# Kernel optimization log

Measured on AMD Instinct MI355X. Metric: run time of the kernel, lower is better.

## Reference

```python
import jax, jax.numpy as jnp
import numpy as np

B, T, D, H, FF = 4, 2048, 768, 12, 4
DH = D // H


def _ln(x, g, b, eps=1e-5):
    mu = x.mean(-1, keepdims=True)
    var = ((x - mu) ** 2).mean(-1, keepdims=True)
    return (x - mu) * jax.lax.rsqrt(var + eps) * g + b


def setup_inputs() -> dict:
    key = jax.random.key(0)
    ks = jax.random.split(key, 16)
    s = 0.02
    d = {
        'x': jax.random.normal(ks[0], (B, T, D), jnp.float32),
        'Wq': jax.random.normal(ks[1], (D, D), jnp.float32) * s,
        'bq': jnp.zeros((D,), jnp.float32),
        'Wk': jax.random.normal(ks[2], (D, D), jnp.float32) * s,
        'bk': jnp.zeros((D,), jnp.float32),
        'Wv': jax.random.normal(ks[3], (D, D), jnp.float32) * s,
        'bv': jnp.zeros((D,), jnp.float32),
        'Wo': jax.random.normal(ks[4], (D, D), jnp.float32) * s,
        'bo': jnp.zeros((D,), jnp.float32),
        'W1': jax.random.normal(ks[5], (D, D * FF), jnp.float32) * s,
        'b1': jnp.zeros((D * FF,), jnp.float32),
        'W2': jax.random.normal(ks[6], (D * FF, D), jnp.float32) * s,
        'b2': jnp.zeros((D,), jnp.float32),
        'g1': jnp.ones((D,), jnp.float32),
        'be1': jnp.zeros((D,), jnp.float32),
        'g2': jnp.ones((D,), jnp.float32),
        'be2': jnp.zeros((D,), jnp.float32),
        'radius': 64,
    }
    return d


def reference(x, Wq, bq, Wk, bk, Wv, bv, Wo, bo, W1, b1, W2, b2, g1, be1, g2, be2, radius):
    Bc, Tc, Dc = x.shape
    # local mask: blocked (True) where |i-j| > radius (clamping in torch code is a no-op)
    i = jnp.arange(Tc)
    mask = jnp.abs(i[:, None] - i[None, :]) > radius  # [T,T] True = masked

    h = _ln(x, g1, be1)
    q = (h @ Wq + bq).reshape(Bc, Tc, H, DH)
    k = (h @ Wk + bk).reshape(Bc, Tc, H, DH)
    v = (h @ Wv + bv).reshape(Bc, Tc, H, DH)
    scale = 1.0 / jnp.sqrt(jnp.asarray(DH, x.dtype))
    scores = jnp.einsum('bthd,bshd->bhts', q, k) * scale  # [B,H,T,T]
    scores = jnp.where(mask[None, None], -jnp.inf, scores)
    attn = jax.nn.softmax(scores, axis=-1)
    ctx = jnp.einsum('bhts,bshd->bthd', attn, v).reshape(Bc, Tc, Dc)
    x = x + (ctx @ Wo + bo)

    h2 = _ln(x, g2, be2)
    ff = jax.nn.gelu(h2 @ W1 + b1, approximate=False) @ W2 + b2
    return x + ff
```

## Files before the change

### kernel.cpp

```cpp
#include <hip/hip_runtime.h>
#include <hip/hip_bf16.h>

#define B_  4
#define T_  2048
#define D_  768
#define H_  12
#define DH_ 64
#define FF_ 3072

typedef __attribute__((ext_vector_type(8))) short bf16x8;
typedef __attribute__((ext_vector_type(4))) float f32x4;
typedef __attribute__((ext_vector_type(4))) unsigned short us4;

#define MFMA16(a, b, c) __builtin_amdgcn_mfma_f32_16x16x32_bf16((a), (b), (c), 0, 0, 0)

__device__ __forceinline__ unsigned short f2bf(float f) {
    union { float f; unsigned u; } v; v.f = f;
    unsigned r = v.u + 0x7fffu + ((v.u >> 16) & 1u);
    return (unsigned short)(r >> 16);
}
__device__ __forceinline__ float bf2f(unsigned short s) {
    union { unsigned u; float f; } v; v.u = ((unsigned)s) << 16;
    return v.f;
}

__device__ __forceinline__ float gelu_fast(float v) {
    const float u2 = 2.0f * v * fmaf(0.0356774081f, v * v, 0.7978845608f);
    const float e = __expf(u2);
    const float r = __builtin_amdgcn_rcpf(e + 1.0f);
    const float th = fmaf(-2.0f, r, 1.0f);
    return 0.5f * v * (1.0f + th);
}

__device__ __forceinline__ void gload_lds16(const unsigned short* gp, unsigned short* lp) {
    __builtin_amdgcn_global_load_lds(
        (const __attribute__((address_space(1))) unsigned int*)gp,
        (__attribute__((address_space(3))) unsigned int*)lp,
        16, 0, 0);
}

__global__ __launch_bounds__(256) void tcvt_kernel(
    const float* __restrict__ src, unsigned short* __restrict__ dst, int K, int N)
{
    __shared__ float tile[32][33];
    const int bx = blockIdx.x * 32;
    const int by = blockIdx.y * 32;
    const int tx = threadIdx.x, ty = threadIdx.y;
#pragma unroll
    for (int i = 0; i < 32; i += 8)
        tile[ty + i][tx] = src[(size_t)(by + ty + i) * N + bx + tx];
    __syncthreads();
#pragma unroll
    for (int i = 0; i < 32; i += 8)
        dst[(size_t)(bx + ty + i) * K + by + tx] = f2bf(tile[tx][ty + i]);
}

__global__ __launch_bounds__(256) void tcvt4_kernel(
    const float* __restrict__ s0, const float* __restrict__ s1,
    const float* __restrict__ s2, const float* __restrict__ s3,
    unsigned short* __restrict__ dst)
{
    __shared__ float tile[32][33];
    const int z = blockIdx.z;
    const float* src = (z == 0) ? s0 : (z == 1) ? s1 : (z == 2) ? s2 : s3;
    unsigned short* d = dst + (size_t)z * 589824;
    const int bx = blockIdx.x * 32;
    const int by = blockIdx.y * 32;
    const int tx = threadIdx.x, ty = threadIdx.y;
#pragma unroll
    for (int i = 0; i < 32; i += 8)
        tile[ty + i][tx] = src[(size_t)(by + ty + i) * 768 + bx + tx];
    __syncthreads();
#pragma unroll
    for (int i = 0; i < 32; i += 8)
        d[(size_t)(bx + ty + i) * 768 + by + tx] = f2bf(tile[tx][ty + i]);
}

__global__ __launch_bounds__(256) void ln_kernel(
    const float* __restrict__ x, const float* __restrict__ g,
    const float* __restrict__ be, unsigned short* __restrict__ out)
{
    const int lane = threadIdx.x & 63;
    const int row = blockIdx.x * 4 + (threadIdx.x >> 6);
    const float4* xr = (const float4*)(x + (size_t)row * D_);
    float4 v0 = xr[lane], v1 = xr[lane + 64], v2 = xr[lane + 128];
    float s  = v0.x + v0.y + v0.z + v0.w + v1.x + v1.y + v1.z + v1.w
             + v2.x + v2.y + v2.z + v2.w;
    float s2 = v0.x*v0.x + v0.y*v0.y + v0.z*v0.z + v0.w*v0.w
             + v1.x*v1.x + v1.y*v1.y + v1.z*v1.z + v1.w*v1.w
             + v2.x*v2.x + v2.y*v2.y + v2.z*v2.z + v2.w*v2.w;
#pragma unroll
    for (int o = 1; o < 64; o <<= 1) {
        s  += __shfl_xor(s,  o);
        s2 += __shfl_xor(s2, o);
    }
    const float mu = s * (1.0f / D_);
    const float var = s2 * (1.0f / D_) - mu * mu;
    const float rstd = rsqrtf(var + 1e-5f);
    const float4* gv = (const float4*)g;
    const float4* bv = (const float4*)be;
    us4* orow = (us4*)(out + (size_t)row * D_);
#pragma unroll
    for (int k = 0; k < 3; ++k) {
        const float4 v = (k == 0) ? v0 : (k == 1) ? v1 : v2;
        const float4 gg = gv[lane + k * 64];
        const float4 bb = bv[lane + k * 64];
        us4 p;
        p[0] = f2bf((v.x - mu) * rstd * gg.x + bb.x);
        p[1] = f2bf((v.y - mu) * rstd * gg.y + bb.y);
        p[2] = f2bf((v.z - mu) * rstd * gg.z + bb.z);
        p[3] = f2bf((v.w - mu) * rstd * gg.w + bb.w);
        orow[lane + k * 64] = p;
    }
}

__global__ __launch_bounds__(256) void reduce_ln_kernel(
    const unsigned short* __restrict__ p0, const unsigned short* __restrict__ p1,
    const float* __restrict__ x, const float* __restrict__ bo,
    const float* __restrict__ g, const float* __restrict__ be,
    float* __restrict__ x2, unsigned short* __restrict__ h2)
{
    const int row = blockIdx.x;
    const int t = threadIdx.x;
    const size_t base = (size_t)row * D_;
    float v[3];
    float s = 0.0f, s2 = 0.0f;
#pragma unroll
    for (int j = 0; j < 3; ++j) {
        const int c = t + j * 256;
        const float vv = bf2f(p0[base + c]) + bf2f(p1[base + c]) + bo[c] + x[base + c];
        v[j] = vv;
        x2[base + c] = vv;
        s += vv; s2 += vv * vv;
    }
#pragma unroll
    for (int o = 1; o < 64; o <<= 1) {
        s  += __shfl_xor(s,  o);
        s2 += __shfl_xor(s2, o);
    }
    __shared__ float rs[4], rq[4];
    const int wave = t >> 6;
    if ((t & 63) == 0) { rs[wave] = s; rq[wave] = s2; }
    __syncthreads();
    s  = rs[0] + rs[1] + rs[2] + rs[3];
    s2 = rq[0] + rq[1] + rq[2] + rq[3];
    const float mu = s * (1.0f / D_);
    const float var = s2 * (1.0f / D_) - mu * mu;
    const float rstd = rsqrtf(var + 1e-5f);
#pragma unroll
    for (int j = 0; j < 3; ++j) {
        const int c = t + j * 256;
        h2[base + c] = f2bf((v[j] - mu) * rstd * g[c] + be[c]);
    }
}

__global__ __launch_bounds__(256) void reduce_out_kernel(
    const unsigned short* __restrict__ p0, const unsigned short* __restrict__ p1,
    const float* __restrict__ x2, const float* __restrict__ b2,
    float* __restrict__ out)
{
    const int n4 = B_ * T_ * D_ / 4;
    for (int i = blockIdx.x * 256 + threadIdx.x; i < n4; i += gridDim.x * 256) {
        const us4 a = ((const us4*)p0)[i];
        const us4 b = ((const us4*)p1)[i];
        const float4 xr = ((const float4*)x2)[i];
        const int col = (i * 4) % D_;
        float4 o;
        o.x = bf2f(a[0]) + bf2f(b[0]) + b2[col]     + xr.x;
        o.y = bf2f(a[1]) + bf2f(b[1]) + b2[col + 1] + xr.y;
        o.z = bf2f(a[2]) + bf2f(b[2]) + b2[col + 2] + xr.z;
        o.w = bf2f(a[3]) + bf2f(b[3]) + b2[col + 3] + xr.w;
        ((float4*)out)[i] = o;
    }
}

template<int MODE>
__global__ __launch_bounds__(256, 3) void gemm4w(
    const unsigned short* __restrict__ A,
    const unsigned short* __restrict__ Bt,
    const float* __restrict__ bias,
    const float* __restrict__ bias2,
    const float* __restrict__ bias3,
    void* __restrict__ outp,
    void* __restrict__ out2,
    void* __restrict__ out3,
    int N, int K, int kLen, int nTilesN, int nTilesMN, long partStride)
{
    __shared__ __align__(16) unsigned short As[128 * 64];
    __shared__ __align__(16) unsigned short Bs[128 * 64];

    const int nwg = gridDim.x;
    const int q = nwg >> 3, rr = nwg & 7;
    const int xcd = blockIdx.x & 7, loc = blockIdx.x >> 3;
    const int swz = (xcd < rr ? xcd * (q + 1) : rr * (q + 1) + (xcd - rr) * q) + loc;
    const int ks  = swz / nTilesMN;
    const int rem = swz - ks * nTilesMN;
    const int m0 = (rem / nTilesN) * 128;
    const int n0 = (rem % nTilesN) * 128;
    const int kOff = ks * kLen;

    const int tid = threadIdx.x;
    const int wv = tid >> 6;
    const int lane = tid & 63;
    const int wr = wv >> 1;
    const int wc = wv & 1;

    f32x4 zero4 = {0.0f, 0.0f, 0.0f, 0.0f};
    f32x4 acc[4][4];
#pragma unroll
    for (int i = 0; i < 4; ++i)
#pragma unroll
        for (int j = 0; j < 4; ++j) acc[i][j] = zero4;

    const int lrow = lane >> 3;
    const int scb = (lane & 7) ^ lrow;
    const unsigned short* ag = A  + (size_t)(m0 + wv * 32 + lrow) * K + kOff + scb * 8;
    const unsigned short* bg = Bt + (size_t)(n0 + wv * 32 + lrow) * K + kOff + scb * 8;
    unsigned short* aLds = As + wv * 32 * 64;
    unsigned short* bLds = Bs + wv * 32 * 64;

    const int fr = lane & 15;
    const int fg = lane >> 4;
    const int sw = fr & 7;
    const int aRow = (wr * 64 + fr) * 64;
    const int bRow = (wc * 64 + fr) * 64;

    const int nk = kLen >> 6;
    for (int kt = 0; kt < nk; ++kt) {
        const int k0 = kt << 6;
        __syncthreads();
#pragma unroll
        for (int c = 0; c < 4; ++c)
            gload_lds16(ag + k0 + (size_t)c * 8 * K, aLds + c * 512);
#pragma unroll
        for (int c = 0; c < 4; ++c)
            gload_lds16(bg + k0 + (size_t)c * 8 * K, bLds + c * 512);
        __syncthreads();

#pragma unroll
        for (int kk = 0; kk < 2; ++kk) {
            bf16x8 afr[4], bfr[4];
            const int cb = ((kk * 4 + fg) ^ sw) << 3;
#pragma unroll
            for (int mm = 0; mm < 4; ++mm)
                afr[mm] = *(const bf16x8*)(As + aRow + mm * 1024 + cb);
#pragma unroll
            for (int nn = 0; nn < 4; ++nn)
                bfr[nn] = *(const bf16x8*)(Bs + bRow + nn * 1024 + cb);
#pragma unroll
            for (int mm = 0; mm < 4; ++mm)
#pragma unroll
                for (int nn = 0; nn < 4; ++nn)
                    acc[mm][nn] = MFMA16(afr[mm], bfr[nn], acc[mm][nn]);
        }
    }

    const int lc = lane & 15;
    const int lr = (lane >> 4) * 4;
#pragma unroll
    for (int mm = 0; mm < 4; ++mm) {
        const int gm0 = m0 + wr * 64 + mm * 16 + lr;
#pragma unroll
        for (int nn = 0; nn < 4; ++nn) {
            const int gn = n0 + wc * 64 + nn * 16 + lc;
            if (MODE == 4) {
                if (gn < 1536) {
                    const float bv = (gn < 768) ? bias[gn] : bias2[gn - 768];
                    unsigned short* o = (gn < 768) ? (unsigned short*)outp : (unsigned short*)out2;
                    const int col = (gn < 768) ? gn : gn - 768;
#pragma unroll
                    for (int r = 0; r < 4; ++r)
                        o[(size_t)(gm0 + r) * 768 + col] = f2bf(acc[mm][nn][r] + bv);
                } else {
                    const float bv = bias3[gn - 1536];
                    const int b = gm0 / T_;
                    const int tl = gm0 - b * T_;
                    us4 pk;
#pragma unroll
                    for (int r = 0; r < 4; ++r) pk[r] = f2bf(acc[mm][nn][r] + bv);
                    *(us4*)((unsigned short*)out3 + ((size_t)(b * D_ + gn - 1536)) * T_ + tl) = pk;
                }
            } else if (MODE == 5) {
                unsigned short* o = (unsigned short*)outp + (size_t)ks * partStride;
#pragma unroll
                for (int r = 0; r < 4; ++r)
                    o[(size_t)(gm0 + r) * N + gn] = f2bf(acc[mm][nn][r]);
            } else {
                const float bv = bias[gn];
#pragma unroll
                for (int r = 0; r < 4; ++r) {
                    const int gm = gm0 + r;
                    float v = acc[mm][nn][r] + bv;
                    if (MODE == 0) {
                        ((unsigned short*)outp)[(size_t)gm * N + gn] = f2bf(v);
                    } else if (MODE == 2) {
                        ((unsigned short*)outp)[(size_t)gm * N + gn] = f2bf(gelu_fast(v));
                    }
                }
            }
        }
    }
}

__global__ __launch_bounds__(256) void attn_kernel(
    const unsigned short* __restrict__ Q,
    const unsigned short* __restrict__ Kg,
    const unsigned short* __restrict__ Vt,
    unsigned short* __restrict__ ctx)
{
    __shared__ __align__(16) unsigned short Qs[64][72];
    __shared__ __align__(16) unsigned short KP[192 * 72];
    __shared__ __align__(16) unsigned short Vts[64][200];

    const int tid = threadIdx.x;
    const int lane = tid & 63;
    const int w = tid >> 6;
    const int bid = blockIdx.x;
    const int qt = bid & 31;
    const int h = (bid >> 5) % H_;
    const int b = bid / (32 * H_);
    const int qs = qt * 64;
    const int t0 = qs >= 64 ? qs - 64 : 0;
    const int t1 = (qs + 128 < T_) ? qs + 128 : T_;
    const int KW = t1 - t0;

    for (int s = tid; s < 512; s += 256) {
        const int r = s >> 3, c8 = (s & 7) << 3;
        *(uint4*)&Qs[r][c8] =
            *(const uint4*)&Q[((size_t)(b * T_ + qs + r)) * D_ + h * DH_ + c8];
    }
    unsigned short* Ks = KP;
    for (int s = tid; s < 1536; s += 256) {
        const int r = s >> 3, c8 = (s & 7) << 3;
        uint4 val = {0, 0, 0, 0};
        if (r < KW)
            val = *(const uint4*)&Kg[((size_t)(b * T_ + t0 + r)) * D_ + h * DH_ + c8];
        *(uint4*)&Ks[r * 72 + c8] = val;
    }
    for (int s = tid; s < 1536; s += 256) {
        const int r = s / 24, c8 = (s % 24) << 3;
        uint4 val = {0, 0, 0, 0};
        if (c8 < KW)
            val = *(const uint4*)&Vt[((size_t)((b * H_ + h) * DH_ + r)) * T_ + t0 + c8];
        *(uint4*)&Vts[r][c8] = val;
    }
    __syncthreads();

    f32x4 zero4 = {0.0f, 0.0f, 0.0f, 0.0f};
    f32x4 sa[12];
#pragma unroll
    for (int i = 0; i < 12; ++i) sa[i] = zero4;
#pragma unroll
    for (int ks = 0; ks < 2; ++ks) {
        const bf16x8 aq = *(const bf16x8*)&Qs[w * 16 + (lane & 15)][ks * 32 + (lane >> 4) * 8];
#pragma unroll
        for (int cf = 0; cf < 12; ++cf) {
            const bf16x8 bk = *(const bf16x8*)&Ks[(cf * 16 + (lane & 15)) * 72 + ks * 32 + (lane >> 4) * 8];
            sa[cf] = MFMA16(aq, bk, sa[cf]);
        }
    }
    __syncthreads();

    const int lq = w * 16 + (lane >> 4) * 4;
    float mx[4] = {-1e30f, -1e30f, -1e30f, -1e30f};
#pragma unroll
    for (int cf = 0; cf < 12; ++cf) {
        const int key = t0 + cf * 16 + (lane & 15);
#pragma unroll
        for (int r = 0; r < 4; ++r) {
            const int dd = (qs + lq + r) - key;
            const bool ok = (key < t1) && (dd <= 64) && (dd >= -64);
            const float sv = ok ? sa[cf][r] * 0.125f : -1e30f;
            sa[cf][r] = sv;
            mx[r] = fmaxf(mx[r], sv);
        }
    }
#pragma unroll
    for (int r = 0; r < 4; ++r)
#pragma unroll
        for (int o = 1; o < 16; o <<= 1)
            mx[r] = fmaxf(mx[r], __shfl_xor(mx[r], o));

    unsigned short* Ps = KP;
    float sm[4] = {0.0f, 0.0f, 0.0f, 0.0f};
#pragma unroll
    for (int cf = 0; cf < 12; ++cf) {
#pragma unroll
        for (int r = 0; r < 4; ++r) {
            const float p = __expf(sa[cf][r] - mx[r]);
            sm[r] += p;
            Ps[(lq + r) * 200 + cf * 16 + (lane & 15)] = f2bf(p);
        }
    }
#pragma unroll
    for (int r = 0; r < 4; ++r)
#pragma unroll
        for (int o = 1; o < 16; o <<= 1)
            sm[r] += __shfl_xor(sm[r], o);

    f32x4 oa[4];
#pragma unroll
    for (int i = 0; i < 4; ++i) oa[i] = zero4;
#pragma unroll
    for (int ks = 0; ks < 6; ++ks) {
        const bf16x8 ap = *(const bf16x8*)&Ps[(w * 16 + (lane & 15)) * 200 + ks * 32 + (lane >> 4) * 8];
#pragma unroll
        for (int nf = 0; nf < 4; ++nf) {
            const bf16x8 bv = *(const bf16x8*)&Vts[nf * 16 + (lane & 15)][ks * 32 + (lane >> 4) * 8];
            oa[nf] = MFMA16(ap, bv, oa[nf]);
        }
    }
#pragma unroll
    for (int nf = 0; nf < 4; ++nf) {
#pragma unroll
        for (int r = 0; r < 4; ++r) {
            const float o = oa[nf][r] / sm[r];
            ctx[((size_t)(b * T_ + qs + lq + r)) * D_ + h * DH_ + nf * 16 + (lane & 15)] = f2bf(o);
        }
    }
}

extern "C" void kernel_launch(void* const* d_in, const int* in_sizes, int n_in,
                              void* d_out, int out_size, void* d_ws, size_t ws_size,
                              hipStream_t stream)
{
    const float* x   = (const float*)d_in[0];
    const float* Wq  = (const float*)d_in[1];
    const float* bq  = (const float*)d_in[2];
    const float* Wk  = (const float*)d_in[3];
    const float* bk  = (const float*)d_in[4];
    const float* Wv  = (const float*)d_in[5];
    const float* bv  = (const float*)d_in[6];
    const float* Wo  = (const float*)d_in[7];
    const float* bo  = (const float*)d_in[8];
    const float* W1  = (const float*)d_in[9];
    const float* b1  = (const float*)d_in[10];
    const float* W2  = (const float*)d_in[11];
    const float* b2  = (const float*)d_in[12];
    const float* g1  = (const float*)d_in[13];
    const float* be1 = (const float*)d_in[14];
    const float* g2  = (const float*)d_in[15];
    const float* be2 = (const float*)d_in[16];
    float* out = (float*)d_out;

    unsigned short* wqkv_t = (unsigned short*)d_ws;
    unsigned short* wo_t = wqkv_t + 3 * 589824;
    unsigned short* w1_t = wo_t + 589824;
    unsigned short* w2_t = w1_t + 2359296;
    unsigned short* hbuf = w2_t + 2359296;
    unsigned short* qbuf = hbuf + 6291456;
    float* x2 = (float*)(qbuf + 6291456);
    unsigned short* kbuf = (unsigned short*)(x2 + 6291456);
    unsigned short* vtb  = kbuf + 6291456;
    unsigned short* ffb  = kbuf;

    dim3 tb(32, 8);
    tcvt4_kernel<<<dim3(24, 24, 4), tb, 0, stream>>>(Wq, Wk, Wv, Wo, wqkv_t);
    tcvt_kernel<<<dim3(96, 24), tb, 0, stream>>>(W1, w1_t, 768, 3072);
    tcvt_kernel<<<dim3(24, 96), tb, 0, stream>>>(W2, w2_t, 3072, 768);

    ln_kernel<<<2048, 256, 0, stream>>>(x, g1, be1, hbuf);

    gemm4w<4><<<64 * 18, 256, 0, stream>>>(
        hbuf, wqkv_t, bq, bk, bv, qbuf, kbuf, vtb, 2304, 768, 768, 18, 64 * 18, 0);

    attn_kernel<<<1536, 256, 0, stream>>>(qbuf, kbuf, vtb, hbuf);

    gemm4w<5><<<64 * 6 * 2, 256, 0, stream>>>(
        hbuf, wo_t, nullptr, nullptr, nullptr, kbuf, nullptr, nullptr,
        768, 768, 384, 6, 64 * 6, 6291456);

    reduce_ln_kernel<<<8192, 256, 0, stream>>>(
        kbuf, kbuf + 6291456, x, bo, g2, be2, x2, qbuf);

    gemm4w<2><<<64 * 24, 256, 0, stream>>>(
        qbuf, w1_t, b1, nullptr, nullptr, ffb, nullptr, nullptr,
        3072, 768, 768, 24, 64 * 24, 0);

    gemm4w<5><<<64 * 6 * 2, 256, 0, stream>>>(
        ffb, w2_t, nullptr, nullptr, nullptr, hbuf, nullptr, nullptr,
        768, 3072, 1536, 6, 64 * 6, 6291456);

    reduce_out_kernel<<<2048, 256, 0, stream>>>(
        hbuf, hbuf + 6291456, x2, b2, out);
}
```

Measured before the change: 230.7 us.

## Store residual in bf16, vectorize reduce-LN per wave, stage V transpose through LDS

The post-attention reduce+LayerNorm kernel now handles one row per wave with vectorized loads and stores, and drops the cross-wave shared-memory reduction. The intermediate residual x2 is stored as bf16 instead of fp32, which halves its write and read traffic in both reduce kernels. In the QKV GEMM, the V-transpose epilogue stages tiles in swizzled LDS so it can write coalesced 16-byte rows, replacing scattered 8-byte stores. Storing the residual in bf16 loses precision in the final output's residual path.

Result: faster. 223.1 us (-3.3%).

```diff
diff --git a/kernel.cpp b/kernel.cpp
--- a/kernel.cpp
+++ b/kernel.cpp
@@ -11,6 +11,7 @@
 typedef __attribute__((ext_vector_type(8))) short bf16x8;
 typedef __attribute__((ext_vector_type(4))) float f32x4;
 typedef __attribute__((ext_vector_type(4))) unsigned short us4;
+typedef __attribute__((ext_vector_type(8))) unsigned short us8;
 
 #define MFMA16(a, b, c) __builtin_amdgcn_mfma_f32_16x16x32_bf16((a), (b), (c), 0, 0, 0)
 
@@ -118,58 +119,70 @@
     const unsigned short* __restrict__ p0, const unsigned short* __restrict__ p1,
     const float* __restrict__ x, const float* __restrict__ bo,
     const float* __restrict__ g, const float* __restrict__ be,
-    float* __restrict__ x2, unsigned short* __restrict__ h2)
-{
-    const int row = blockIdx.x;
-    const int t = threadIdx.x;
+    unsigned short* __restrict__ x2, unsigned short* __restrict__ h2)
+{
+    const int lane = threadIdx.x & 63;
+    const int row = blockIdx.x * 4 + (threadIdx.x >> 6);
     const size_t base = (size_t)row * D_;
-    float v[3];
+    float v[12];
     float s = 0.0f, s2 = 0.0f;
 #pragma unroll
-    for (int j = 0; j < 3; ++j) {
-        const int c = t + j * 256;
-        const float vv = bf2f(p0[base + c]) + bf2f(p1[base + c]) + bo[c] + x[base + c];
-        v[j] = vv;
-        x2[base + c] = vv;
-        s += vv; s2 += vv * vv;
+    for (int k = 0; k < 3; ++k) {
+        const int c = k * 256 + lane * 4;
+        const us4 a = *(const us4*)(p0 + base + c);
+        const us4 b = *(const us4*)(p1 + base + c);
+        const float4 xr = *(const float4*)(x + base + c);
+        const float4 bb = *(const float4*)(bo + c);
+        const float w0 = bf2f(a[0]) + bf2f(b[0]) + bb.x + xr.x;
+        const float w1 = bf2f(a[1]) + bf2f(b[1]) + bb.y + xr.y;
+        const float w2 = bf2f(a[2]) + bf2f(b[2]) + bb.z + xr.z;
+        const float w3 = bf2f(a[3]) + bf2f(b[3]) + bb.w + xr.w;
+        v[k * 4 + 0] = w0; v[k * 4 + 1] = w1; v[k * 4 + 2] = w2; v[k * 4 + 3] = w3;
+        s += w0 + w1 + w2 + w3;
+        s2 += w0 * w0 + w1 * w1 + w2 * w2 + w3 * w3;
     }
 #pragma unroll
     for (int o = 1; o < 64; o <<= 1) {
         s  += __shfl_xor(s,  o);
         s2 += __shfl_xor(s2, o);
     }
-    __shared__ float rs[4], rq[4];
-    const int wave = t >> 6;
-    if ((t & 63) == 0) { rs[wave] = s; rq[wave] = s2; }
-    __syncthreads();
-    s  = rs[0] + rs[1] + rs[2] + rs[3];
-    s2 = rq[0] + rq[1] + rq[2] + rq[3];
     const float mu = s * (1.0f / D_);
     const float var = s2 * (1.0f / D_) - mu * mu;
     const float rstd = rsqrtf(var + 1e-5f);
 #pragma unroll
-    for (int j = 0; j < 3; ++j) {
-        const int c = t + j * 256;
-        h2[base + c] = f2bf((v[j] - mu) * rstd * g[c] + be[c]);
+    for (int k = 0; k < 3; ++k) {
+        const int c = k * 256 + lane * 4;
+        const float4 gg = *(const float4*)(g + c);
+        const float4 bb = *(const float4*)(be + c);
+        us4 xo, ho;
+        xo[0] = f2bf(v[k*4+0]); xo[1] = f2bf(v[k*4+1]);
+        xo[2] = f2bf(v[k*4+2]); xo[3] = f2bf(v[k*4+3]);
+        ho[0] = f2bf((v[k*4+0] - mu) * rstd * gg.x + bb.x);
+        ho[1] = f2bf((v[k*4+1] - mu) * rstd * gg.y + bb.y);
+        ho[2] = f2bf((v[k*4+2] - mu) * rstd * gg.z + bb.z);
+        ho[3] = f2bf((v[k*4+3] - mu) * rstd * gg.w + bb.w);
+        *(us4*)(x2 + base + c) = xo;
+        *(us4*)(h2 + base + c) = ho;
     }
 }
 
 __global__ __launch_bounds__(256) void reduce_out_kernel(
     const unsigned short* __restrict__ p0, const unsigned short* __restrict__ p1,
-    const float* __restrict__ x2, const float* __restrict__ b2,
+    const unsigned short* __restrict__ x2, const float* __restrict__ b2,
     float* __restrict__ out)
 {
     const int n4 = B_ * T_ * D_ / 4;
     for (int i = blockIdx.x * 256 + threadIdx.x; i < n4; i += gridDim.x * 256) {
         const us4 a = ((const us4*)p0)[i];
         const us4 b = ((const us4*)p1)[i];
-        const float4 xr = ((const float4*)x2)[i];
+        const us4 xr = ((const us4*)x2)[i];
         const int col = (i * 4) % D_;
+        const float4 bb = *(const float4*)(b2 + col);
         float4 o;
-        o.x = bf2f(a[0]) + bf2f(b[0]) + b2[col]     + xr.x;
-        o.y = bf2f(a[1]) + bf2f(b[1]) + b2[col + 1] + xr.y;
-        o.z = bf2f(a[2]) + bf2f(b[2]) + b2[col + 2] + xr.z;
-        o.w = bf2f(a[3]) + bf2f(b[3]) + b2[col + 3] + xr.w;
+        o.x = bf2f(a[0]) + bf2f(b[0]) + bb.x + bf2f(xr[0]);
+        o.y = bf2f(a[1]) + bf2f(b[1]) + bb.y + bf2f(xr[1]);
+        o.z = bf2f(a[2]) + bf2f(b[2]) + bb.z + bf2f(xr[2]);
+        o.w = bf2f(a[3]) + bf2f(b[3]) + bb.w + bf2f(xr[3]);
         ((float4*)out)[i] = o;
     }
 }
@@ -257,6 +270,39 @@
 
     const int lc = lane & 15;
     const int lr = (lane >> 4) * 4;
+
+    if (MODE == 4 && n0 >= 1536) {
+        __syncthreads();
+        unsigned short* Vl = As + wv * 4096;
+#pragma unroll
+        for (int mm = 0; mm < 4; ++mm) {
+            const int s = mm * 4 + (lane >> 4);
+            const int sp = s >> 1, so = s & 1;
+#pragma unroll
+            for (int nn = 0; nn < 4; ++nn) {
+                const int d = nn * 16 + lc;
+                const float bv = bias3[(n0 - 1536) + wc * 64 + d];
+                us4 pk;
+#pragma unroll
+                for (int r = 0; r < 4; ++r) pk[r] = f2bf(acc[mm][nn][r] + bv);
+                *(us4*)(Vl + d * 64 + ((sp ^ (d & 7)) << 3) + so * 4) = pk;
+            }
+        }
+        asm volatile("s_waitcnt lgkmcnt(0)" ::: "memory");
+        const int bb = m0 >> 11;
+        const int tl0 = (m0 & 2047) + wr * 64;
+        const size_t rowbase = (size_t)(bb * D_ + (n0 - 1536) + wc * 64);
+        unsigned short* vout = (unsigned short*)out3;
+#pragma unroll
+        for (int it = 0; it < 8; ++it) {
+            const int d = (lane >> 3) + it * 8;
+            const int c = lane & 7;
+            const us8 v = *(const us8*)(Vl + d * 64 + ((c ^ (d & 7)) << 3));
+            *(us8*)(vout + (rowbase + d) * (size_t)T_ + tl0 + c * 8) = v;
+        }
+        return;
+    }
+
 #pragma unroll
     for (int mm = 0; mm < 4; ++mm) {
         const int gm0 = m0 + wr * 64 + mm * 16 + lr;
@@ -264,22 +310,13 @@
         for (int nn = 0; nn < 4; ++nn) {
             const int gn = n0 + wc * 64 + nn * 16 + lc;
             if (MODE == 4) {
-                if (gn < 1536) {
-                    const float bv = (gn < 768) ? bias[gn] : bias2[gn - 768];
-                    unsigned short* o = (gn < 768) ? (unsigned short*)outp : (unsigned short*)out2;
-                    const int col = (gn < 768) ? gn : gn - 768;
-#pragma unroll
-                    for (int r = 0; r < 4; ++r)
-                        o[(size_t)(gm0 + r) * 768 + col] = f2bf(acc[mm][nn][r] + bv);
-                } else {
-                    const float bv = bias3[gn - 1536];
-                    const int b = gm0 / T_;
-                    const int tl = gm0 - b * T_;
-                    us4 pk;
-#pragma unroll
-                    for (int r = 0; r < 4; ++r) pk[r] = f2bf(acc[mm][nn][r] + bv);
-                    *(us4*)((unsigned short*)out3 + ((size_t)(b * D_ + gn - 1536)) * T_ + tl) = pk;
-                }
+                const bool isQ = (n0 < 768);
+                unsigned short* o = isQ ? (unsigned short*)outp : (unsigned short*)out2;
+                const int col = isQ ? gn : gn - 768;
+                const float bv = isQ ? bias[col] : bias2[col];
+#pragma unroll
+                for (int r = 0; r < 4; ++r)
+                    o[(size_t)(gm0 + r) * 768 + col] = f2bf(acc[mm][nn][r] + bv);
             } else if (MODE == 5) {
                 unsigned short* o = (unsigned short*)outp + (size_t)ks * partStride;
 #pragma unroll
@@ -449,8 +486,8 @@
     unsigned short* w2_t = w1_t + 2359296;
     unsigned short* hbuf = w2_t + 2359296;
     unsigned short* qbuf = hbuf + 6291456;
-    float* x2 = (float*)(qbuf + 6291456);
-    unsigned short* kbuf = (unsigned short*)(x2 + 6291456);
+    unsigned short* x2b  = qbuf + 6291456;
+    unsigned short* kbuf = x2b + 2 * 6291456;
     unsigned short* vtb  = kbuf + 6291456;
     unsigned short* ffb  = kbuf;
 
@@ -470,8 +507,8 @@
         hbuf, wo_t, nullptr, nullptr, nullptr, kbuf, nullptr, nullptr,
         768, 768, 384, 6, 64 * 6, 6291456);
 
-    reduce_ln_kernel<<<8192, 256, 0, stream>>>(
-        kbuf, kbuf + 6291456, x, bo, g2, be2, x2, qbuf);
+    reduce_ln_kernel<<<2048, 256, 0, stream>>>(
+        kbuf, kbuf + 6291456, x, bo, g2, be2, x2b, qbuf);
 
     gemm4w<2><<<64 * 24, 256, 0, stream>>>(
         qbuf, w1_t, b1, nullptr, nullptr, ffb, nullptr, nullptr,
@@ -482,5 +519,5 @@
         768, 3072, 1536, 6, 64 * 6, 6291456);
 
     reduce_out_kernel<<<2048, 256, 0, stream>>>(
-        hbuf, hbuf + 6291456, x2, b2, out);
-}
+        hbuf, hbuf + 6291456, x2b, b2, out);
+}
```
